# Optimization experiments

Measured on AMD Instinct MI355X. Metric: run time of the kernel, lower is better.

The kernel has to match this reference:

```python
import jax, jax.numpy as jnp
import numpy as np
from jax import lax


def _pixel_shuffle2(y):
    # torch.nn.PixelShuffle(2): (B, C*4, H, W) -> (B, C, 2H, 2W)
    B, C4, H, W = y.shape
    C = C4 // 4
    y = y.reshape(B, C, 2, 2, H, W)
    y = y.transpose(0, 1, 4, 2, 5, 3)  # B, C, H, r, W, r
    return y.reshape(B, C, H * 2, W * 2)


def setup_inputs() -> dict:
    key = jax.random.key(0)
    k1, k2, k3 = jax.random.split(key, 3)
    n_feat = 96
    x = jax.random.normal(k1, (8, n_feat, 128, 128), dtype=jnp.float32)
    # Conv2d(n_feat, n_feat*2, 3, bias=False); fan-in scaled init
    conv_w = jax.random.normal(k2, (n_feat * 2, n_feat, 3, 3), dtype=jnp.float32) * (1.0 / np.sqrt(n_feat * 9))
    beta = jnp.float32(0.3)
    return {"x": x, "conv_w": conv_w, "beta": beta}


def reference(x, conv_w, beta):
    # conv 3x3 stride 1 pad 1, no bias
    y = lax.conv_general_dilated(
        x, conv_w, window_strides=(1, 1), padding=((1, 1), (1, 1)),
        dimension_numbers=("NCHW", "OIHW", "NCHW"))
    y = _pixel_shuffle2(y)  # (B, n_feat/2, 2H, 2W)
    H2, W2 = y.shape[2], y.shape[3]
    # forward-normalized 2D FFT; torch fftshift with no dim shifts ALL axes
    freq = jnp.fft.fftshift(jnp.fft.fft2(y.astype(jnp.complex64), norm="forward"))
    # crop central low-frequency band (half-size in each spatial dim)
    low = freq[:, :, H2 // 4: H2 // 4 * 3, W2 // 4: W2 // 4 * 3]
    # F.pad(low, (H2//4, H2//4, W2//4, W2//4)): last dim padded by H2//4, dim -2 by W2//4
    low = jnp.pad(low, ((0, 0), (0, 0), (W2 // 4, W2 // 4), (H2 // 4, H2 // 4)))
    low = jnp.abs(jnp.fft.ifft2(jnp.fft.ifftshift(low), norm="forward")).astype(x.dtype)
    high = y - low
    return (1.0 - beta) * low + beta * high
```

## Files before the change

kernel.cpp:

```cpp
#include <hip/hip_runtime.h>
#include <hip/hip_fp16.h>
#include <math.h>

#define PI_F 3.14159265358979f

typedef __attribute__((ext_vector_type(8))) __bf16 bf16x8;
typedef __attribute__((ext_vector_type(4))) float f32x4;

__device__ __forceinline__ unsigned short f2bf_rne(float v) {
  union { float f; unsigned u; } c; c.f = v;
  unsigned u = c.u;
  return (unsigned short)((u + 0x7fffu + ((u >> 16) & 1u)) >> 16);
}
__device__ __forceinline__ float bfbits2f(unsigned short b) {
  union { unsigned u; float f; } c; c.u = ((unsigned)b) << 16; return c.f;
}
__device__ __forceinline__ unsigned pk2(float a, float b) {
  return (unsigned)f2bf_rne(a) | ((unsigned)f2bf_rne(b) << 16);
}

__global__ void prep_w(const float* __restrict__ w, unsigned short* __restrict__ wpk) {
  int i = blockIdx.x * 256 + threadIdx.x;
  if (i >= 9 * 192 * 96) return;
  int pos = i / (192 * 96);
  int rem = i - pos * (192 * 96);
  int oc = rem / 96, ic = rem - oc * 96;
  float v = w[(size_t)rem * 9 + pos];
  unsigned short h = f2bf_rne(v);
  unsigned short l = f2bf_rne(v - bfbits2f(h));
  int q = ic >> 3, j = ic & 7;
  size_t base = ((size_t)(pos * 192 + oc) * 12 + q) * 16;
  wpk[base + j] = h;
  wpk[base + 8 + j] = l;
}

#define ICP 40

__global__ __launch_bounds__(256)
void conv_mfma(const float* __restrict__ x, const unsigned short* __restrict__ wpk,
               float* __restrict__ y) {
  __shared__ unsigned short patch[4 * 66 * ICP];
  const int tid  = threadIdx.x;
  const int wave = tid >> 6, lane = tid & 63;
  const int col  = lane & 15, quad = lane >> 4;
  const int w0 = blockIdx.x * 64;
  const int h0 = blockIdx.y * 2;
  const int b  = blockIdx.z;
  const float* xb = x + (size_t)b * 96 * 128 * 128;

  f32x4 acc[2][3][4];
#pragma unroll
  for (int hh = 0; hh < 2; ++hh)
#pragma unroll
    for (int mt = 0; mt < 3; ++mt)
#pragma unroll
      for (int nt = 0; nt < 4; ++nt) acc[hh][mt][nt] = (f32x4)0.f;

  const int wbase = (48 * wave + col) * 192 + quad * 16;
  const int cg = tid & 15, pg = tid >> 4;
  const int hside = tid & 1, hrr = (tid >> 1) & 3, hicl = tid >> 3;
  const int hgr = h0 - 1 + hrr;
  const int hgc = hside ? (w0 + 64) : (w0 - 1);

  float4 sv0[2], sv1[2];
  float hv;
  auto ISSUE = [&](int phase) {
    const int ic0 = phase * 32;
#pragma unroll
    for (int it = 0; it < 2; ++it) {
      int pairid = it * 16 + pg;
      int r   = pairid & 3;
      int icl = (pairid >> 2) * 2;
      int gr  = h0 - 1 + r;
      const float* r0p = xb + (size_t)(ic0 + icl) * 16384 + gr * 128 + w0 + 4 * cg;
      sv0[it] = make_float4(0.f, 0.f, 0.f, 0.f);
      sv1[it] = sv0[it];
      if ((unsigned)gr < 128u) {
        sv0[it] = *(const float4*)(r0p);
        sv1[it] = *(const float4*)(r0p + 16384);
      }
    }
    hv = 0.f;
    if ((unsigned)hgr < 128u && (unsigned)hgc < 128u)
      hv = xb[(size_t)(ic0 + hicl) * 16384 + hgr * 128 + hgc];
  };
  float4 tv0[2], tv1[2];
  auto ISSUE2 = [&](int phase) {
    const int ic0 = phase * 32;
#pragma unroll
    for (int it = 0; it < 2; ++it) {
      int pairid = 32 + it * 16 + pg;
      int r   = pairid & 3;
      int icl = (pairid >> 2) * 2;
      int gr  = h0 - 1 + r;
      const float* r0p = xb + (size_t)(ic0 + icl) * 16384 + gr * 128 + w0 + 4 * cg;
      tv0[it] = make_float4(0.f, 0.f, 0.f, 0.f);
      tv1[it] = tv0[it];
      if ((unsigned)gr < 128u) {
        tv0[it] = *(const float4*)(r0p);
        tv1[it] = *(const float4*)(r0p + 16384);
      }
    }
  };
  auto WRITE = [&]() {
#pragma unroll
    for (int it = 0; it < 2; ++it) {
      int pairid = it * 16 + pg;
      int r   = pairid & 3;
      int icl = (pairid >> 2) * 2;
      unsigned* pb = (unsigned*)&patch[(r * 66 + 1 + 4 * cg) * ICP + icl];
      pb[0]           = pk2(sv0[it].x, sv1[it].x);
      pb[ICP / 2]     = pk2(sv0[it].y, sv1[it].y);
      pb[ICP]         = pk2(sv0[it].z, sv1[it].z);
      pb[3 * ICP / 2] = pk2(sv0[it].w, sv1[it].w);
    }
#pragma unroll
    for (int it = 0; it < 2; ++it) {
      int pairid = 32 + it * 16 + pg;
      int r   = pairid & 3;
      int icl = (pairid >> 2) * 2;
      unsigned* pb = (unsigned*)&patch[(r * 66 + 1 + 4 * cg) * ICP + icl];
      pb[0]           = pk2(tv0[it].x, tv1[it].x);
      pb[ICP / 2]     = pk2(tv0[it].y, tv1[it].y);
      pb[ICP]         = pk2(tv0[it].z, tv1[it].z);
      pb[3 * ICP / 2] = pk2(tv0[it].w, tv1[it].w);
    }
    patch[(hrr * 66 + (hside ? 65 : 0)) * ICP + hicl] = f2bf_rne(hv);
  };

  ISSUE(0); ISSUE2(0);
  WRITE();
  __syncthreads();

  for (int phase = 0; phase < 3; ++phase) {
    if (phase < 2) { ISSUE(phase + 1); ISSUE2(phase + 1); }

#pragma unroll
    for (int pos = 0; pos < 9; ++pos) {
      const int dy = pos / 3, dx = pos - 3 * dy;
      bf16x8 ah[3], al[3];
#pragma unroll
      for (int mt = 0; mt < 3; ++mt) {
        const unsigned short* wp_ =
            wpk + wbase + (((pos * 192 + mt * 16) * 12 + phase * 4) * 16);
        ah[mt] = *(const bf16x8*)(wp_);
        al[mt] = *(const bf16x8*)(wp_ + 8);
      }
#pragma unroll
      for (int hh = 0; hh < 2; ++hh) {
        bf16x8 bfrag[4];
#pragma unroll
        for (int nt = 0; nt < 4; ++nt)
          bfrag[nt] = *(const bf16x8*)&patch[((dy + hh) * 66 + nt * 16 + col + dx) * ICP + quad * 8];
#pragma unroll
        for (int mt = 0; mt < 3; ++mt)
#pragma unroll
          for (int nt = 0; nt < 4; ++nt) {
            acc[hh][mt][nt] = __builtin_amdgcn_mfma_f32_16x16x32_bf16(ah[mt], bfrag[nt], acc[hh][mt][nt], 0, 0, 0);
            acc[hh][mt][nt] = __builtin_amdgcn_mfma_f32_16x16x32_bf16(al[mt], bfrag[nt], acc[hh][mt][nt], 0, 0, 0);
          }
      }
    }

    if (phase < 2) {
      __syncthreads();
      WRITE();
      __syncthreads();
    }
  }

  float* yb = y + (size_t)b * 48 * 65536;
#pragma unroll
  for (int hh = 0; hh < 2; ++hh) {
    const int h = h0 + hh;
#pragma unroll
    for (int mt = 0; mt < 3; ++mt) {
#pragma unroll
      for (int p = 0; p < 2; ++p) {
        int r0 = 2 * p;
        int oc = 48 * wave + mt * 16 + quad * 4 + r0;
        int cq = oc >> 2, r2 = (oc >> 1) & 1;
        float* orow = yb + ((size_t)cq * 256 + 2 * h + r2) * 256;
#pragma unroll
        for (int nt = 0; nt < 4; ++nt) {
          int w = w0 + nt * 16 + col;
          *(float2*)&orow[2 * w] = make_float2(acc[hh][mt][nt][r0], acc[hh][mt][nt][r0 + 1]);
        }
      }
    }
  }
}

#define OCB 8
#define ICB 2
#define PSTRIDE 67
__global__ __launch_bounds__(256)
void conv_ps_kernel(const float* __restrict__ x, const float* __restrict__ wgt,
                    float* __restrict__ y) {
  __shared__ float wsh[OCB * 96 * 9];
  __shared__ float patch[ICB * 18 * PSTRIDE];
  const int tid = threadIdx.x;
  const int b = blockIdx.z / 24, ocg = blockIdx.z % 24;
  const int row0 = blockIdx.y * 16, col0 = blockIdx.x * 64;
  const int tx = tid & 15, ty = tid >> 4;
  for (int i = tid; i < OCB * 96 * 9; i += 256) wsh[i] = wgt[ocg * (OCB * 96 * 9) + i];
  float acc[OCB][4];
#pragma unroll
  for (int o = 0; o < OCB; ++o)
#pragma unroll
    for (int p = 0; p < 4; ++p) acc[o][p] = 0.f;
  const float* xb = x + (size_t)b * 96 * 128 * 128;
  for (int ic0 = 0; ic0 < 96; ic0 += ICB) {
    __syncthreads();
    for (int idx = tid; idx < ICB * 18 * 66; idx += 256) {
      int j = idx / (18 * 66), rem = idx - j * (18 * 66);
      int r = rem / 66, c = rem - r * 66;
      int gr = row0 - 1 + r, gc = col0 - 1 + c;
      float v = 0.f;
      if ((unsigned)gr < 128u && (unsigned)gc < 128u)
        v = xb[((size_t)(ic0 + j) * 128 + gr) * 128 + gc];
      patch[j * (18 * PSTRIDE) + r * PSTRIDE + c] = v;
    }
    __syncthreads();
#pragma unroll
    for (int j = 0; j < ICB; ++j) {
      float xr[3][6];
      const float* pp = &patch[j * (18 * PSTRIDE) + ty * PSTRIDE + tx * 4];
#pragma unroll
      for (int dy = 0; dy < 3; ++dy)
#pragma unroll
        for (int dx = 0; dx < 6; ++dx) xr[dy][dx] = pp[dy * PSTRIDE + dx];
#pragma unroll
      for (int o = 0; o < OCB; ++o) {
        const float* wp = &wsh[(o * 96 + ic0 + j) * 9];
#pragma unroll
        for (int p = 0; p < 4; ++p)
          acc[o][p] += wp[0] * xr[0][p] + wp[1] * xr[0][p + 1] + wp[2] * xr[0][p + 2]
                     + wp[3] * xr[1][p] + wp[4] * xr[1][p + 1] + wp[5] * xr[1][p + 2]
                     + wp[6] * xr[2][p] + wp[7] * xr[2][p + 1] + wp[8] * xr[2][p + 2];
      }
    }
  }
  const int h = row0 + ty;
#pragma unroll
  for (int o = 0; o < OCB; ++o) {
    int ocglob = ocg * OCB + o;
    int cq = ocglob >> 2, r2 = (ocglob >> 1) & 1, s2 = ocglob & 1;
    float* orow = y + (((size_t)b * 48 + cq) * 256 + (2 * h + r2)) * 256;
#pragma unroll
    for (int p = 0; p < 4; ++p) orow[2 * (col0 + tx * 4 + p) + s2] = acc[o][p];
  }
}

__device__ __forceinline__ float2 cadd(float2 a, float2 b){return make_float2(a.x+b.x, a.y+b.y);}
__device__ __forceinline__ float2 csub(float2 a, float2 b){return make_float2(a.x-b.x, a.y-b.y);}
__device__ __forceinline__ float2 cmul(float2 a, float2 b){return make_float2(a.x*b.x-a.y*b.y, a.x*b.y+a.y*b.x);}
__device__ __forceinline__ float2 cmulc(float2 a, float2 b){return make_float2(a.x*b.x+a.y*b.y, a.y*b.x-a.x*b.y);}

__device__ __forceinline__ void dft4(float2 r[4]) {
  float2 e0 = cadd(r[0], r[2]), e1 = csub(r[0], r[2]);
  float2 o0 = cadd(r[1], r[3]), o1 = csub(r[1], r[3]);
  r[0] = cadd(e0, o0);
  r[2] = csub(e0, o0);
  r[1] = make_float2(e1.x + o1.y, e1.y - o1.x);
  r[3] = make_float2(e1.x - o1.y, e1.y + o1.x);
}
__device__ __forceinline__ void idft4(float2 r[4]) {
  float2 e0 = cadd(r[0], r[2]), e1 = csub(r[0], r[2]);
  float2 o0 = cadd(r[1], r[3]), o1 = csub(r[1], r[3]);
  r[0] = cadd(e0, o0);
  r[2] = csub(e0, o0);
  r[1] = make_float2(e1.x - o1.y, e1.y + o1.x);
  r[3] = make_float2(e1.x + o1.y, e1.y - o1.x);
}

struct TwSet {
  float2 f1[3], f2[3], f3[3], i2[4], i3[4];
};

__device__ __forceinline__ void load_tw(TwSet& T, const float2* __restrict__ tw, int l) {
  const int qq = l >> 4, m = l & 15, q2r = (l >> 2) & 3, c2 = l & 3;
  T.f1[0] = tw[l];
  T.f1[1] = tw[(2 * l) & 255];
  T.f1[2] = tw[(3 * l) & 255];
  T.f2[0] = tw[(4 * m) & 255];
  T.f2[1] = tw[(8 * m) & 255];
  T.f2[2] = tw[(12 * m) & 255];
  T.f3[0] = tw[(16 * c2) & 255];
  T.f3[1] = tw[(32 * c2) & 255];
  T.f3[2] = tw[(48 * c2) & 255];
  T.i2[0] = tw[(4 * c2 * q2r) & 255];
  T.i2[1] = tw[(4 * (c2 + 4) * q2r) & 255];
  T.i2[2] = tw[(4 * (c2 + 8) * q2r) & 255];
  T.i2[3] = tw[(4 * (c2 + 12) * q2r) & 255];
  T.i3[0] = tw[(m * qq) & 255];
  T.i3[1] = tw[((m + 16) * qq) & 255];
  T.i3[2] = tw[((m + 32) * qq) & 255];
  T.i3[3] = tw[((m + 48) * qq) & 255];
}

template <int ST>
__device__ void fft_line_masked(float2 r[4], float2* __restrict__ S, const TwSet& T, int l) {
  const int qq = l >> 4, m = l & 15;
  const int g = l >> 2, q2r = (l >> 2) & 3, c2 = l & 3;
  dft4(r);
  r[1] = cmul(r[1], T.f1[0]);
  r[2] = cmul(r[2], T.f1[1]);
  r[3] = cmul(r[3], T.f1[2]);
  S[ST * l] = r[0];
  S[ST * (64 + l)] = r[1];
  S[ST * (128 + l)] = r[2];
  S[ST * (192 + l)] = r[3];
#pragma unroll
  for (int t = 0; t < 4; ++t) r[t] = S[ST * (qq * 64 + m + 16 * t)];
  dft4(r);
  r[1] = cmul(r[1], T.f2[0]);
  r[2] = cmul(r[2], T.f2[1]);
  r[3] = cmul(r[3], T.f2[2]);
#pragma unroll
  for (int q2 = 0; q2 < 4; ++q2) S[ST * (qq * 64 + q2 * 16 + ((m + 4 * q2) & 15))] = r[q2];
#pragma unroll
  for (int t = 0; t < 4; ++t) r[t] = S[ST * (qq * 64 + q2r * 16 + ((c2 + 4 * t + 4 * q2r) & 15))];
  dft4(r);
  r[1] = cmul(r[1], T.f3[0]);
  r[2] = cmul(r[2], T.f3[1]);
  r[3] = cmul(r[3], T.f3[2]);
#pragma unroll
  for (int q3 = 0; q3 < 4; ++q3) S[ST * (g * 16 + ((4 * q3 + c2 + g) & 15))] = r[q3];
#pragma unroll
  for (int t = 0; t < 4; ++t) r[t] = S[ST * (g * 16 + ((4 * c2 + t + g) & 15))];
  dft4(r);
  {
    float2 V0 = r[0], V3 = r[3];
    r[0] = cadd(V0, V3);
    r[1] = make_float2(V0.x + V3.y, V0.y - V3.x);
    r[2] = csub(V0, V3);
    r[3] = make_float2(V0.x - V3.y, V0.y + V3.x);
  }
  r[1] = cmulc(r[1], T.f3[0]);
  r[2] = cmulc(r[2], T.f3[1]);
  r[3] = cmulc(r[3], T.f3[2]);
#pragma unroll
  for (int j = 0; j < 4; ++j) S[ST * (g * 16 + ((4 * c2 + j + g) & 15))] = r[j];
#pragma unroll
  for (int t = 0; t < 4; ++t) r[t] = S[ST * (g * 16 + ((4 * t + c2 + g) & 15))];
  idft4(r);
  r[0] = cmulc(r[0], T.i2[0]);
  r[1] = cmulc(r[1], T.i2[1]);
  r[2] = cmulc(r[2], T.i2[2]);
  r[3] = cmulc(r[3], T.i2[3]);
#pragma unroll
  for (int t1 = 0; t1 < 4; ++t1) S[ST * (qq * 64 + q2r * 16 + ((c2 + 4 * t1 + 4 * q2r) & 15))] = r[t1];
#pragma unroll
  for (int t = 0; t < 4; ++t) r[t] = S[ST * (qq * 64 + t * 16 + ((m + 4 * t) & 15))];
  idft4(r);
  r[0] = cmulc(r[0], T.i3[0]);
  r[1] = cmulc(r[1], T.i3[1]);
  r[2] = cmulc(r[2], T.i3[2]);
  r[3] = cmulc(r[3], T.i3[3]);
#pragma unroll
  for (int t2 = 0; t2 < 4; ++t2) S[ST * (qq * 64 + m + 16 * t2)] = r[t2];
#pragma unroll
  for (int t = 0; t < 4; ++t) r[t] = S[ST * (t * 64 + l)];
  idft4(r);
}

__global__ __launch_bounds__(256)
void fft_rows_kernel(const float* __restrict__ y, unsigned* __restrict__ z1) {
  __shared__ float2 S[4 * 256];
  __shared__ float2 tw[256];
  const int tid = threadIdx.x;
  {
    float sn, cs;
    __sincosf(-2.f * PI_F * (float)tid / 256.f, &sn, &cs);
    tw[tid] = make_float2(cs, sn);
  }
  __syncthreads();
  const int wv = tid >> 6, l = tid & 63;
  TwSet T;
  load_tw(T, tw, l);
  const size_t rowbase = ((size_t)blockIdx.x * 4 + wv) * 256;
  float2 r[4];
#pragma unroll
  for (int t = 0; t < 4; ++t) r[t] = make_float2(y[rowbase + l + 64 * t], 0.f);
  fft_line_masked<1>(r, S + wv * 256, T, l);
#pragma unroll
  for (int t = 0; t < 4; ++t) {
    __half2 h = __floats2half2_rn(r[t].x * (1.f / 256.f), r[t].y * (1.f / 256.f));
    z1[rowbase + l + 64 * t] = *reinterpret_cast<unsigned*>(&h);
  }
}

#define CST 17
__global__ __launch_bounds__(256)
void fft_cols_kernel(const unsigned* __restrict__ z1, const float* __restrict__ yy,
                     float* __restrict__ out, const float* __restrict__ betaPtr) {
  __shared__ float2 strip[256 * CST];
  __shared__ float2 tw[256];
  const int tid = threadIdx.x;
  {
    float sn, cs;
    __sincosf(-2.f * PI_F * (float)tid / 256.f, &sn, &cs);
    tw[tid] = make_float2(cs, sn);
  }
  const int img = blockIdx.x >> 4;
  const int c0 = (blockIdx.x & 15) * 16;
  const size_t ibase = (size_t)img * 65536;
#pragma unroll
  for (int it = 0; it < 16; ++it) {
    int idx = it * 256 + tid;
    int rrow = idx >> 4, cc = idx & 15;
    unsigned u = z1[ibase + (size_t)rrow * 256 + c0 + cc];
    __half2 h = *reinterpret_cast<__half2*>(&u);
    strip[rrow * CST + cc] = __half22float2(h);
  }
  __syncthreads();
  const int wv = tid >> 6, l = tid & 63;
  TwSet T;
  load_tw(T, tw, l);
  float2 r[4];
#pragma unroll
  for (int ci = 0; ci < 4; ++ci) {
    const int c = wv * 4 + ci;
    float2* Sc = strip + c;
#pragma unroll
    for (int t = 0; t < 4; ++t) r[t] = Sc[CST * (l + 64 * t)];
    fft_line_masked<CST>(r, Sc, T, l);
#pragma unroll
    for (int t = 0; t < 4; ++t) {
      float2 v = r[t];
      Sc[CST * (l + 64 * t)].x = sqrtf(v.x * v.x + v.y * v.y) * (1.f / 256.f);
    }
  }
  __syncthreads();
  const float beta = betaPtr[0];
  const float a1 = 1.f - 2.f * beta;
#pragma unroll
  for (int it = 0; it < 16; ++it) {
    int idx = it * 256 + tid;
    int rrow = idx >> 4, cc = idx & 15;
    size_t gi = ibase + (size_t)rrow * 256 + c0 + cc;
    out[gi] = beta * yy[gi] + a1 * strip[rrow * CST + cc].x;
  }
}

extern "C" void kernel_launch(void* const* d_in, const int* in_sizes, int n_in,
                              void* d_out, int out_size, void* d_ws, size_t ws_size,
                              hipStream_t stream) {
  const float* x = (const float*)d_in[0];
  const float* wgt = (const float*)d_in[1];
  const float* beta = (const float*)d_in[2];
  float* out = (float*)d_out;

  const size_t wplane = (size_t)9 * 192 * 96;
  const size_t wbytes = (2 * wplane * sizeof(unsigned short) + 255) & ~(size_t)255;
  const size_t per_img = 65536ull * sizeof(unsigned);
  const int NIMG = 8 * 48;

  unsigned* z1;
  size_t z1_bytes;

  if (ws_size >= wbytes + per_img) {
    unsigned short* wpk = (unsigned short*)d_ws;
    z1 = (unsigned*)((char*)d_ws + wbytes);
    z1_bytes = ws_size - wbytes;
    prep_w<<<648, 256, 0, stream>>>(wgt, wpk);
    conv_mfma<<<dim3(2, 64, 8), 256, 0, stream>>>(x, wpk, out);
  } else {
    z1 = (unsigned*)d_ws;
    z1_bytes = ws_size;
    conv_ps_kernel<<<dim3(2, 8, 192), 256, 0, stream>>>(x, wgt, out);
  }

  int chunk = (int)(z1_bytes / per_img);
  if (chunk < 1) chunk = 1;
  if (chunk > NIMG) chunk = NIMG;
  for (int img0 = 0; img0 < NIMG; img0 += chunk) {
    int n = NIMG - img0;
    if (n > chunk) n = chunk;
    float* ych = out + (size_t)img0 * 65536;
    fft_rows_kernel<<<n * 64, 256, 0, stream>>>(ych, z1);
    fft_cols_kernel<<<n * 16, 256, 0, stream>>>(z1, ych, ych, beta);
  }
}
```

Baseline: 358.9 us.

## Pack two real rows per complex FFT and store half-width real intermediates

The row pass now packs two real rows into one complex 256-point FFT, which halves the number of row FFTs. The separated spectra are stored as single half-precision reals instead of half2 complex values, so the intermediate buffer is half the size. Correction terms at the masked-band boundaries are computed with wave reductions, transformed by a small auxiliary FFT kernel, and added back in the column pass. The column pass also handles two columns per complex FFT. The cost is an extra kernel launch, more intricate correction arithmetic, and precision risk from the packed representation.

```diff
diff --git a/kernel.cpp b/kernel.cpp
--- a/kernel.cpp
+++ b/kernel.cpp
@@ -256,6 +256,22 @@
 __device__ __forceinline__ float2 csub(float2 a, float2 b){return make_float2(a.x-b.x, a.y-b.y);}
 __device__ __forceinline__ float2 cmul(float2 a, float2 b){return make_float2(a.x*b.x-a.y*b.y, a.x*b.y+a.y*b.x);}
 __device__ __forceinline__ float2 cmulc(float2 a, float2 b){return make_float2(a.x*b.x+a.y*b.y, a.y*b.x-a.x*b.y);}
+
+__device__ __forceinline__ float2 ipow(int m) {
+  m &= 3;
+  float2 v;
+  v.x = (m == 0) ? 1.f : ((m == 2) ? -1.f : 0.f);
+  v.y = (m == 1) ? 1.f : ((m == 3) ? -1.f : 0.f);
+  return v;
+}
+__device__ __forceinline__ float2 wave_sum(float2 v) {
+#pragma unroll
+  for (int off = 32; off; off >>= 1) {
+    v.x += __shfl_xor(v.x, off);
+    v.y += __shfl_xor(v.y, off);
+  }
+  return v;
+}
 
 __device__ __forceinline__ void dft4(float2 r[4]) {
   float2 e0 = cadd(r[0], r[2]), e1 = csub(r[0], r[2]);
@@ -366,7 +382,8 @@
 }
 
 __global__ __launch_bounds__(256)
-void fft_rows_kernel(const float* __restrict__ y, unsigned* __restrict__ z1) {
+void fft_rows_kernel(const float* __restrict__ y, __half* __restrict__ z1,
+                     float2* __restrict__ cvec) {
   __shared__ float2 S[4 * 256];
   __shared__ float2 tw[256];
   const int tid = threadIdx.x;
@@ -379,23 +396,37 @@
   const int wv = tid >> 6, l = tid & 63;
   TwSet T;
   load_tw(T, tw, l);
-  const size_t rowbase = ((size_t)blockIdx.x * 4 + wv) * 256;
+  const int pair = blockIdx.x * 4 + wv;
+  const size_t abase = (size_t)pair * 512;
   float2 r[4];
 #pragma unroll
-  for (int t = 0; t < 4; ++t) r[t] = make_float2(y[rowbase + l + 64 * t], 0.f);
+  for (int t = 0; t < 4; ++t)
+    r[t] = make_float2(y[abase + l + 64 * t], y[abase + 256 + l + 64 * t]);
+  float2 s = cadd(cadd(r[0], r[1]), cadd(r[2], r[3]));
+  float2 Z64  = wave_sum(cmul(s, tw[(64 * l) & 255]));
+  float2 Z192 = wave_sum(cmul(s, tw[(192 * l) & 255]));
   fft_line_masked<1>(r, S + wv * 256, T, l);
+  const float2 u = ipow(l);
+  const float2 zu = cmul(Z64, u);
 #pragma unroll
   for (int t = 0; t < 4; ++t) {
-    __half2 h = __floats2half2_rn(r[t].x * (1.f / 256.f), r[t].y * (1.f / 256.f));
-    z1[rowbase + l + 64 * t] = *reinterpret_cast<unsigned*>(&h);
-  }
-}
-
-#define CST 17
+    float2 gS = cadd(r[t], zu);
+    z1[abase + l + 64 * t]       = __float2half_rn(gS.x * (1.f / 256.f));
+    z1[abase + 256 + l + 64 * t] = __float2half_rn(gS.y * (1.f / 256.f));
+  }
+  if (l == 0) {
+    float2 cj = make_float2(Z192.x, -Z192.y);
+    float2 A = make_float2(0.5f * (Z64.x + cj.x), 0.5f * (Z64.y + cj.y));
+    float2 q = make_float2(Z64.x - cj.x, Z64.y - cj.y);
+    float2 B = make_float2(0.5f * q.y, -0.5f * q.x);
+    cvec[2 * pair]     = make_float2(-A.x * (1.f / 256.f), -A.y * (1.f / 256.f));
+    cvec[2 * pair + 1] = make_float2(-B.x * (1.f / 256.f), -B.y * (1.f / 256.f));
+  }
+}
+
 __global__ __launch_bounds__(256)
-void fft_cols_kernel(const unsigned* __restrict__ z1, const float* __restrict__ yy,
-                     float* __restrict__ out, const float* __restrict__ betaPtr) {
-  __shared__ float2 strip[256 * CST];
+void fft_aux_kernel(const float2* __restrict__ cvec, float2* __restrict__ Mc, int nimg) {
+  __shared__ float2 S[4 * 256];
   __shared__ float2 tw[256];
   const int tid = threadIdx.x;
   {
@@ -403,33 +434,83 @@
     __sincosf(-2.f * PI_F * (float)tid / 256.f, &sn, &cs);
     tw[tid] = make_float2(cs, sn);
   }
+  __syncthreads();
+  const int wv = tid >> 6, l = tid & 63;
+  const int img = blockIdx.x * 4 + wv;
+  TwSet T;
+  load_tw(T, tw, l);
+  if (img >= nimg) return;
+  float2 r[4];
+#pragma unroll
+  for (int t = 0; t < 4; ++t) r[t] = cvec[(size_t)img * 256 + l + 64 * t];
+  fft_line_masked<1>(r, S + wv * 256, T, l);
+#pragma unroll
+  for (int t = 0; t < 4; ++t) Mc[(size_t)img * 256 + l + 64 * t] = r[t];
+}
+
+#define CSTF 17
+__global__ __launch_bounds__(256)
+void fft_cols_kernel(const __half* __restrict__ z1, const float2* __restrict__ Mc,
+                     const float* __restrict__ yy, float* __restrict__ out,
+                     const float* __restrict__ betaPtr) {
+  __shared__ float strip[256 * CSTF];
+  __shared__ float2 S2[4 * 256];
+  __shared__ float2 tw[256];
+  __shared__ float2 McS[256];
+  const int tid = threadIdx.x;
+  {
+    float sn, cs;
+    __sincosf(-2.f * PI_F * (float)tid / 256.f, &sn, &cs);
+    tw[tid] = make_float2(cs, sn);
+  }
   const int img = blockIdx.x >> 4;
   const int c0 = (blockIdx.x & 15) * 16;
   const size_t ibase = (size_t)img * 65536;
+  McS[tid] = Mc[(size_t)img * 256 + tid];
 #pragma unroll
   for (int it = 0; it < 16; ++it) {
     int idx = it * 256 + tid;
     int rrow = idx >> 4, cc = idx & 15;
-    unsigned u = z1[ibase + (size_t)rrow * 256 + c0 + cc];
-    __half2 h = *reinterpret_cast<__half2*>(&u);
-    strip[rrow * CST + cc] = __half22float2(h);
+    strip[rrow * CSTF + cc] = __half2float(z1[ibase + (size_t)rrow * 256 + c0 + cc]);
   }
   __syncthreads();
   const int wv = tid >> 6, l = tid & 63;
   TwSet T;
   load_tw(T, tw, l);
+  const float2 u = ipow(l);
   float2 r[4];
 #pragma unroll
-  for (int ci = 0; ci < 4; ++ci) {
-    const int c = wv * 4 + ci;
-    float2* Sc = strip + c;
-#pragma unroll
-    for (int t = 0; t < 4; ++t) r[t] = Sc[CST * (l + 64 * t)];
-    fft_line_masked<CST>(r, Sc, T, l);
+  for (int p = 0; p < 2; ++p) {
+    const int cc = wv * 4 + p * 2;
+    const int wglob = c0 + cc;
 #pragma unroll
     for (int t = 0; t < 4; ++t) {
-      float2 v = r[t];
-      Sc[CST * (l + 64 * t)].x = sqrtf(v.x * v.x + v.y * v.y) * (1.f / 256.f);
+      const float* sp = &strip[(l + 64 * t) * CSTF + cc];
+      r[t] = make_float2(sp[0], sp[1]);
+    }
+    float2 s = cadd(cadd(r[0], r[1]), cadd(r[2], r[3]));
+    float2 Z64  = wave_sum(cmul(s, tw[(64 * l) & 255]));
+    float2 Z192 = wave_sum(cmul(s, tw[(192 * l) & 255]));
+    fft_line_masked<1>(r, S2 + wv * 256, T, l);
+    float2 cj = make_float2(Z192.x, -Z192.y);
+    float2 A = make_float2(0.5f * (Z64.x + cj.x), 0.5f * (Z64.y + cj.y));
+    float2 q = make_float2(Z64.x - cj.x, Z64.y - cj.y);
+    float2 B = make_float2(0.5f * q.y, -0.5f * q.x);
+    const float2 zu = cmul(Z64, u);
+    const float2 Au = cmul(A, u);
+    const float2 Bu = cmul(B, u);
+    const float2 iw  = ipow(wglob);
+    const float2 iw1 = ipow(wglob + 1);
+#pragma unroll
+    for (int t = 0; t < 4; ++t) {
+      int h = l + 64 * t;
+      float2 gS = cadd(r[t], zu);
+      float2 mc  = cmul(McS[h], iw);
+      float2 mc1 = cmul(McS[h], iw1);
+      float2 Fc  = make_float2(gS.x - Au.x + mc.x,  -Au.y + mc.y);
+      float2 Fc1 = make_float2(gS.y - Bu.x + mc1.x, -Bu.y + mc1.y);
+      strip[h * CSTF + cc]     = sqrtf(Fc.x * Fc.x + Fc.y * Fc.y) * (1.f / 256.f);
+      strip[h * CSTF + cc + 1] = sqrtf(Fc1.x * Fc1.x + Fc1.y * Fc1.y) * (1.f / 256.f);
     }
   }
   __syncthreads();
@@ -440,7 +521,7 @@
     int idx = it * 256 + tid;
     int rrow = idx >> 4, cc = idx & 15;
     size_t gi = ibase + (size_t)rrow * 256 + c0 + cc;
-    out[gi] = beta * yy[gi] + a1 * strip[rrow * CST + cc].x;
+    out[gi] = beta * yy[gi] + a1 * strip[rrow * CSTF + cc];
   }
 }
 
@@ -454,32 +535,37 @@
 
   const size_t wplane = (size_t)9 * 192 * 96;
   const size_t wbytes = (2 * wplane * sizeof(unsigned short) + 255) & ~(size_t)255;
-  const size_t per_img = 65536ull * sizeof(unsigned);
+  const size_t per_img = 65536ull * 2 + 256 * 8 + 256 * 8;
   const int NIMG = 8 * 48;
 
-  unsigned* z1;
-  size_t z1_bytes;
+  char* fftws;
+  size_t fft_bytes;
 
   if (ws_size >= wbytes + per_img) {
     unsigned short* wpk = (unsigned short*)d_ws;
-    z1 = (unsigned*)((char*)d_ws + wbytes);
-    z1_bytes = ws_size - wbytes;
+    fftws = (char*)d_ws + wbytes;
+    fft_bytes = ws_size - wbytes;
     prep_w<<<648, 256, 0, stream>>>(wgt, wpk);
     conv_mfma<<<dim3(2, 64, 8), 256, 0, stream>>>(x, wpk, out);
   } else {
-    z1 = (unsigned*)d_ws;
-    z1_bytes = ws_size;
+    fftws = (char*)d_ws;
+    fft_bytes = ws_size;
     conv_ps_kernel<<<dim3(2, 8, 192), 256, 0, stream>>>(x, wgt, out);
   }
 
-  int chunk = (int)(z1_bytes / per_img);
+  int chunk = (int)(fft_bytes / per_img);
   if (chunk < 1) chunk = 1;
   if (chunk > NIMG) chunk = NIMG;
+  __half* z1h = (__half*)fftws;
+  float2* cvec = (float2*)(fftws + (size_t)chunk * 131072);
+  float2* Mc = cvec + (size_t)chunk * 256;
+
   for (int img0 = 0; img0 < NIMG; img0 += chunk) {
     int n = NIMG - img0;
     if (n > chunk) n = chunk;
     float* ych = out + (size_t)img0 * 65536;
-    fft_rows_kernel<<<n * 64, 256, 0, stream>>>(ych, z1);
-    fft_cols_kernel<<<n * 16, 256, 0, stream>>>(z1, ych, ych, beta);
-  }
-}
+    fft_rows_kernel<<<n * 32, 256, 0, stream>>>(ych, z1h, cvec);
+    fft_aux_kernel<<<(n + 3) / 4, 256, 0, stream>>>(cvec, Mc, n);
+    fft_cols_kernel<<<n * 16, 256, 0, stream>>>(z1h, Mc, ych, ych, beta);
+  }
+}
```

Measured after the change: 392.2 us. 9.3% more time.
